# Kernel tuning notes

Hardware: AMD Instinct MI355X
Metric: run time of the kernel (lower is better)

The kernel has to match this reference:

```python
import jax, jax.numpy as jnp
import numpy as np

GAMMA1 = 5.0
GAMMA2 = 5.0
ALPHA = 0.2
BETA = 1.0
K = 0.1
SEQ = 5

B = 16384
EMB = 64
ITEM_NUM = 200000
USER_NUM = 100000
CLUSTER = 64


def setup_inputs() -> dict:
    key = jax.random.key(0)
    ks = jax.random.split(key, 7)
    u = jax.random.randint(ks[0], (B,), 0, USER_NUM)
    X = jax.random.randint(ks[1], (B, SEQ), 0, ITEM_NUM + 1)
    y = jax.random.randint(ks[2], (B,), 0, ITEM_NUM + 1)
    item_emb = jax.random.normal(ks[3], (ITEM_NUM + 1, EMB), dtype=jnp.float32)
    user_emb = jax.random.normal(ks[4], (USER_NUM, EMB), dtype=jnp.float32)
    ae_raw = jax.random.normal(ks[5], (ITEM_NUM + 1, CLUSTER), dtype=jnp.float32)
    w_raw = jax.random.normal(ks[6], (CLUSTER, CLUSTER), dtype=jnp.float32)
    return {"u": u, "X": X, "y": y, "item_emb": item_emb,
            "user_emb": user_emb, "ae_raw": ae_raw, "w_raw": w_raw}


def reference(u, X, y, item_emb, user_emb, ae_raw, w_raw):
    # constructor preprocessing: _handle_ae / _filter_w
    ae = jax.nn.softmax(ae_raw * 10.0 * GAMMA1, axis=1)        # [I+1, C]
    w = jax.nn.softmax(w_raw * 100.0 * GAMMA2, axis=0)          # [C, C]
    # padding_idx=0 -> row 0 of item embedding is zero
    item_emb = item_emb.at[0].set(0.0)

    u_emb = user_emb[u]            # [B, E]
    X_emb = item_emb[X]            # [B, S, E]
    y_emb = item_emb[y]            # [B, E]

    # cluster affinity: ae[X] @ w @ ae[y]
    fac = jnp.einsum('bsc,cd,bd->bs', ae[X], w, ae[y])          # [B, S]

    # time attenuation: [0.6, 0.7, 0.8, 0.9, 1.0]
    time_factor = 1.0 - (SEQ - 1 - jnp.arange(SEQ, dtype=jnp.float32)) * K

    scores = (jnp.einsum('bse,be->bs', X_emb, y_emb)
              * BETA * jnp.exp(fac) * time_factor)              # [B, S]
    z = jax.nn.softmax(scores, axis=1)                          # [B, S]
    p = jnp.einsum('bse,bs->be', X_emb, z)                      # [B, E]
    p_u = p * ALPHA + u_emb                                     # [B, E]
    # diag(sigmoid(p_u @ y_emb.T)) == sigmoid(rowwise dot)
    return jax.nn.sigmoid(jnp.sum(p_u * y_emb, axis=-1))        # [B]
```

## Files before the change

kernel.cpp:

```cpp
#include <hip/hip_runtime.h>
#include <math.h>

#define SEQ 5
#define EMBC 64

typedef float4 f4;

template<int CTRL>
__device__ __forceinline__ float dpp_rot(float v) {
    return __int_as_float(__builtin_amdgcn_update_dpp(
        0, __float_as_int(v), CTRL, 0xF, 0xF, true));
}
__device__ __forceinline__ float sub_sum(float v) {
    v += dpp_rot<0x128>(v);
    v += dpp_rot<0x124>(v);
    v += dpp_rot<0x122>(v);
    v += dpp_rot<0x121>(v);
    return v;
}
__device__ __forceinline__ float sub_max(float v) {
    v = fmaxf(v, dpp_rot<0x128>(v));
    v = fmaxf(v, dpp_rot<0x124>(v));
    v = fmaxf(v, dpp_rot<0x122>(v));
    v = fmaxf(v, dpp_rot<0x121>(v));
    return v;
}
__device__ __forceinline__ float wave_max64(float v) {
    #pragma unroll
    for (int o = 32; o > 0; o >>= 1) v = fmaxf(v, __shfl_xor(v, o, 64));
    return v;
}
__device__ __forceinline__ float wave_sum64(float v) {
    #pragma unroll
    for (int o = 32; o > 0; o >>= 1) v += __shfl_xor(v, o, 64);
    return v;
}
__device__ __forceinline__ float dot4(f4 a, f4 b) {
    return fmaf(a.x, b.x, fmaf(a.y, b.y, fmaf(a.z, b.z, a.w * b.w)));
}
__device__ __forceinline__ f4 fma4(f4 a, float s, f4 c) {
    f4 r; r.x = fmaf(a.x, s, c.x); r.y = fmaf(a.y, s, c.y);
          r.z = fmaf(a.z, s, c.z); r.w = fmaf(a.w, s, c.w); return r;
}
__device__ __forceinline__ f4 sub_softmax(f4 a, float scale) {
    a.x *= scale; a.y *= scale; a.z *= scale; a.w *= scale;
    const float m = sub_max(fmaxf(fmaxf(a.x, a.y), fmaxf(a.z, a.w)));
    f4 e; e.x = __expf(a.x - m); e.y = __expf(a.y - m);
          e.z = __expf(a.z - m); e.w = __expf(a.w - m);
    const float inv = 1.0f / sub_sum(((e.x + e.y) + (e.z + e.w)));
    e.x *= inv; e.y *= inv; e.z *= inv; e.w *= inv;
    return e;
}

__global__ __launch_bounds__(64) void wprep_kernel(
    const float* __restrict__ w_raw, float* __restrict__ wT)
{
    const int d = blockIdx.x;
    const int c = threadIdx.x;
    float x = w_raw[c * EMBC + d] * 500.0f;
    const float m = wave_max64(x);
    const float e = __expf(x - m);
    const float s = wave_sum64(e);
    wT[d * EMBC + c] = e / s;
}

__global__ __launch_bounds__(256) void rumc_main(
    const int* __restrict__ u_idx, const int* __restrict__ X_idx,
    const int* __restrict__ y_idx,
    const float* __restrict__ item_emb, const float* __restrict__ user_emb,
    const float* __restrict__ ae_raw, const float* __restrict__ wT,
    float* __restrict__ out, int B)
{
    __shared__ f4 s_w[EMBC * 16];
    __shared__ f4 s_ae[16 * 16];

    const int t = threadIdx.x;

    #pragma unroll
    for (int i = 0; i < 4; ++i)
        s_w[t + 256 * i] = ((const f4*)wT)[t + 256 * i];

    const int wave = t >> 6;
    const int lane = t & 63;
    const int sub  = lane >> 4;
    const int sl   = lane & 15;
    const int g    = wave * 4 + sub;

    int b = blockIdx.x * 16 + g;
    const bool live = (b < B);
    if (!live) b = B - 1;

    __syncthreads();

    const int yi = y_idx[b];
    const int ui = u_idx[b];
    int xi[SEQ];
    #pragma unroll
    for (int s = 0; s < SEQ; ++s) xi[s] = X_idx[b * SEQ + s];

    const f4* __restrict__ item4 = (const f4*)item_emb;
    const f4* __restrict__ user4 = (const f4*)user_emb;
    const f4* __restrict__ ae4   = (const f4*)ae_raw;

    f4 aey = ae4[yi * 16 + sl];
    f4 ax[SEQ];
    #pragma unroll
    for (int s = 0; s < SEQ; ++s) ax[s] = ae4[xi[s] * 16 + sl];
    f4 ye = item4[yi * 16 + sl];
    f4 xe[SEQ];
    #pragma unroll
    for (int s = 0; s < SEQ; ++s) xe[s] = item4[xi[s] * 16 + sl];
    f4 ue = user4[ui * 16 + sl];

    if (yi == 0) { ye.x = ye.y = ye.z = ye.w = 0.0f; }
    #pragma unroll
    for (int s = 0; s < SEQ; ++s)
        if (xi[s] == 0) { xe[s].x = xe[s].y = xe[s].z = xe[s].w = 0.0f; }

    aey = sub_softmax(aey, 50.0f);
    s_ae[g * 16 + sl] = aey;

    f4 v; v.x = v.y = v.z = v.w = 0.0f;
    #pragma unroll
    for (int dd = 0; dd < 16; ++dd) {
        const f4 a  = s_ae[g * 16 + dd];
        const f4 w0 = s_w[(4 * dd + 0) * 16 + sl];
        const f4 w1 = s_w[(4 * dd + 1) * 16 + sl];
        const f4 w2 = s_w[(4 * dd + 2) * 16 + sl];
        const f4 w3 = s_w[(4 * dd + 3) * 16 + sl];
        v = fma4(w0, a.x, v);
        v = fma4(w1, a.y, v);
        v = fma4(w2, a.z, v);
        v = fma4(w3, a.w, v);
    }

    float sc[SEQ];
    #pragma unroll
    for (int s = 0; s < SEQ; ++s) {
        const f4 a = sub_softmax(ax[s], 50.0f);
        const float fac = sub_sum(dot4(a, v));
        const float dot = sub_sum(dot4(xe[s], ye));
        const float tf = 1.0f - (float)(SEQ - 1 - s) * 0.1f;
        sc[s] = dot * __expf(fac) * tf;
    }

    float ms = sc[0];
    #pragma unroll
    for (int s = 1; s < SEQ; ++s) ms = fmaxf(ms, sc[s]);
    float Z = 0.0f;
    #pragma unroll
    for (int s = 0; s < SEQ; ++s) { sc[s] = __expf(sc[s] - ms); Z += sc[s]; }
    const float invZ = 1.0f / Z;

    f4 p; p.x = p.y = p.z = p.w = 0.0f;
    #pragma unroll
    for (int s = 0; s < SEQ; ++s) p = fma4(xe[s], sc[s] * invZ, p);
    const f4 pu = fma4(p, 0.2f, ue);
    const float fin = sub_sum(dot4(pu, ye));
    if (live && sl == 0)
        out[b] = 1.0f / (1.0f + __expf(-fin));
}

extern "C" void kernel_launch(void* const* d_in, const int* in_sizes, int n_in,
                              void* d_out, int out_size, void* d_ws, size_t ws_size,
                              hipStream_t stream) {
    const int*   u        = (const int*)d_in[0];
    const int*   X        = (const int*)d_in[1];
    const int*   y        = (const int*)d_in[2];
    const float* item_emb = (const float*)d_in[3];
    const float* user_emb = (const float*)d_in[4];
    const float* ae_raw   = (const float*)d_in[5];
    const float* w_raw    = (const float*)d_in[6];
    float*       out      = (float*)d_out;
    float*       wT       = (float*)d_ws;

    const int B = in_sizes[0];
    const int grid = (B + 15) / 16;

    wprep_kernel<<<EMBC, EMBC, 0, stream>>>(w_raw, wT);
    rumc_main<<<grid, 256, 0, stream>>>(u, X, y, item_emb, user_emb,
                                        ae_raw, wT, out, B);
}
```

Baseline: 139.9 us.

## Fuse w softmax preprocessing into main kernel, removing separate prep launch

Drops the separate wprep kernel. Each block now loads raw w into shared memory and computes the column softmax itself, with 4 threads per column and shuffle reductions, writing into a padded (stride-17) shared layout. This removes one kernel launch and the global round trip for wT. In exchange, all 1024 blocks redo the 64x64 softmax, and the kernel uses more shared memory and gains an extra barrier.

```diff
diff --git a/kernel.cpp b/kernel.cpp
--- a/kernel.cpp
+++ b/kernel.cpp
@@ -25,16 +25,6 @@
     v = fmaxf(v, dpp_rot<0x121>(v));
     return v;
 }
-__device__ __forceinline__ float wave_max64(float v) {
-    #pragma unroll
-    for (int o = 32; o > 0; o >>= 1) v = fmaxf(v, __shfl_xor(v, o, 64));
-    return v;
-}
-__device__ __forceinline__ float wave_sum64(float v) {
-    #pragma unroll
-    for (int o = 32; o > 0; o >>= 1) v += __shfl_xor(v, o, 64);
-    return v;
-}
 __device__ __forceinline__ float dot4(f4 a, f4 b) {
     return fmaf(a.x, b.x, fmaf(a.y, b.y, fmaf(a.z, b.z, a.w * b.w)));
 }
@@ -52,33 +42,22 @@
     return e;
 }
 
-__global__ __launch_bounds__(64) void wprep_kernel(
-    const float* __restrict__ w_raw, float* __restrict__ wT)
-{
-    const int d = blockIdx.x;
-    const int c = threadIdx.x;
-    float x = w_raw[c * EMBC + d] * 500.0f;
-    const float m = wave_max64(x);
-    const float e = __expf(x - m);
-    const float s = wave_sum64(e);
-    wT[d * EMBC + c] = e / s;
-}
-
-__global__ __launch_bounds__(256) void rumc_main(
+__global__ __launch_bounds__(256) void rumc_fused(
     const int* __restrict__ u_idx, const int* __restrict__ X_idx,
     const int* __restrict__ y_idx,
     const float* __restrict__ item_emb, const float* __restrict__ user_emb,
-    const float* __restrict__ ae_raw, const float* __restrict__ wT,
+    const float* __restrict__ ae_raw, const float* __restrict__ w_raw,
     float* __restrict__ out, int B)
 {
-    __shared__ f4 s_w[EMBC * 16];
+    __shared__ f4 s_raw[EMBC * 16];
+    __shared__ f4 s_w[EMBC * 17];
     __shared__ f4 s_ae[16 * 16];
 
     const int t = threadIdx.x;
 
     #pragma unroll
     for (int i = 0; i < 4; ++i)
-        s_w[t + 256 * i] = ((const f4*)wT)[t + 256 * i];
+        s_raw[t + 256 * i] = ((const f4*)w_raw)[t + 256 * i];
 
     const int wave = t >> 6;
     const int lane = t & 63;
@@ -90,13 +69,13 @@
     const bool live = (b < B);
     if (!live) b = B - 1;
 
-    __syncthreads();
-
     const int yi = y_idx[b];
     const int ui = u_idx[b];
     int xi[SEQ];
     #pragma unroll
     for (int s = 0; s < SEQ; ++s) xi[s] = X_idx[b * SEQ + s];
+
+    __syncthreads();
 
     const f4* __restrict__ item4 = (const f4*)item_emb;
     const f4* __restrict__ user4 = (const f4*)user_emb;
@@ -106,16 +85,42 @@
     f4 ax[SEQ];
     #pragma unroll
     for (int s = 0; s < SEQ; ++s) ax[s] = ae4[xi[s] * 16 + sl];
+
+    {
+        const int d = t >> 2;
+        const int q = t & 3;
+        const float* __restrict__ sr = (const float*)s_raw;
+        float x[16];
+        #pragma unroll
+        for (int k = 0; k < 16; ++k)
+            x[k] = sr[(q * 16 + k) * EMBC + d] * 500.0f;
+        float m = x[0];
+        #pragma unroll
+        for (int k = 1; k < 16; ++k) m = fmaxf(m, x[k]);
+        m = fmaxf(m, __shfl_xor(m, 1, 64));
+        m = fmaxf(m, __shfl_xor(m, 2, 64));
+        float ssum = 0.0f;
+        #pragma unroll
+        for (int k = 0; k < 16; ++k) { x[k] = __expf(x[k] - m); ssum += x[k]; }
+        ssum += __shfl_xor(ssum, 1, 64);
+        ssum += __shfl_xor(ssum, 2, 64);
+        const float inv = 1.0f / ssum;
+        #pragma unroll
+        for (int i = 0; i < 4; ++i) {
+            f4 wv;
+            wv.x = x[4 * i + 0] * inv; wv.y = x[4 * i + 1] * inv;
+            wv.z = x[4 * i + 2] * inv; wv.w = x[4 * i + 3] * inv;
+            s_w[d * 17 + q * 4 + i] = wv;
+        }
+    }
+
+    __syncthreads();
+
     f4 ye = item4[yi * 16 + sl];
     f4 xe[SEQ];
     #pragma unroll
     for (int s = 0; s < SEQ; ++s) xe[s] = item4[xi[s] * 16 + sl];
     f4 ue = user4[ui * 16 + sl];
-
-    if (yi == 0) { ye.x = ye.y = ye.z = ye.w = 0.0f; }
-    #pragma unroll
-    for (int s = 0; s < SEQ; ++s)
-        if (xi[s] == 0) { xe[s].x = xe[s].y = xe[s].z = xe[s].w = 0.0f; }
 
     aey = sub_softmax(aey, 50.0f);
     s_ae[g * 16 + sl] = aey;
@@ -124,15 +129,20 @@
     #pragma unroll
     for (int dd = 0; dd < 16; ++dd) {
         const f4 a  = s_ae[g * 16 + dd];
-        const f4 w0 = s_w[(4 * dd + 0) * 16 + sl];
-        const f4 w1 = s_w[(4 * dd + 1) * 16 + sl];
-        const f4 w2 = s_w[(4 * dd + 2) * 16 + sl];
-        const f4 w3 = s_w[(4 * dd + 3) * 16 + sl];
+        const f4 w0 = s_w[(4 * dd + 0) * 17 + sl];
+        const f4 w1 = s_w[(4 * dd + 1) * 17 + sl];
+        const f4 w2 = s_w[(4 * dd + 2) * 17 + sl];
+        const f4 w3 = s_w[(4 * dd + 3) * 17 + sl];
         v = fma4(w0, a.x, v);
         v = fma4(w1, a.y, v);
         v = fma4(w2, a.z, v);
         v = fma4(w3, a.w, v);
     }
+
+    if (yi == 0) { ye.x = ye.y = ye.z = ye.w = 0.0f; }
+    #pragma unroll
+    for (int s = 0; s < SEQ; ++s)
+        if (xi[s] == 0) { xe[s].x = xe[s].y = xe[s].z = xe[s].w = 0.0f; }
 
     float sc[SEQ];
     #pragma unroll
@@ -172,12 +182,11 @@
     const float* ae_raw   = (const float*)d_in[5];
     const float* w_raw    = (const float*)d_in[6];
     float*       out      = (float*)d_out;
-    float*       wT       = (float*)d_ws;
+    (void)d_ws; (void)ws_size;
 
     const int B = in_sizes[0];
     const int grid = (B + 15) / 16;
 
-    wprep_kernel<<<EMBC, EMBC, 0, stream>>>(w_raw, wT);
-    rumc_main<<<grid, 256, 0, stream>>>(u, X, y, item_emb, user_emb,
-                                        ae_raw, wT, out, B);
+    rumc_fused<<<grid, 256, 0, stream>>>(u, X, y, item_emb, user_emb,
+                                         ae_raw, w_raw, out, B);
 }
```

Result: no change. 137.8 us (-1.5%).
